# Performance work log

Measured on AMD Instinct MI355X. Metric: run time of the kernel, lower is better.

Reference implementation:

```python
import jax, jax.numpy as jnp
import numpy as np

B, C, H, W = 16, 512, 64, 64
R = 8
CP = C // R  # inner channel dim C' = 64


def setup_inputs() -> dict:
    key = jax.random.key(0)
    ks = jax.random.split(key, 10)
    s_in = 1.0 / np.sqrt(C)
    s_cp = 1.0 / np.sqrt(CP)
    return {
        "x": jax.random.normal(ks[0], (B, C, H, W), dtype=jnp.float32),
        "wq": jax.random.uniform(ks[1], (CP, C), jnp.float32, -s_in, s_in),
        "bq": jax.random.uniform(ks[2], (CP,), jnp.float32, -s_in, s_in),
        "wk": jax.random.uniform(ks[3], (CP, C), jnp.float32, -s_in, s_in),
        "bk": jax.random.uniform(ks[4], (CP,), jnp.float32, -s_in, s_in),
        "wv": jax.random.uniform(ks[5], (CP, C), jnp.float32, -s_in, s_in),
        "bv": jax.random.uniform(ks[6], (CP,), jnp.float32, -s_in, s_in),
        "wo": jax.random.uniform(ks[7], (C, CP), jnp.float32, -s_cp, s_cp),
        "bo": jax.random.uniform(ks[8], (C,), jnp.float32, -s_cp, s_cp),
        # torch init is gamma=0 (output==x, zero grads to convs); use small
        # nonzero value so the reference exercises the full graph.
        "gamma": jax.random.normal(ks[9], (1,), dtype=jnp.float32) * 0.1,
    }


def reference(x, wq, bq, wk, bk, wv, bv, wo, bo, gamma):
    b, c, h, w = x.shape
    n = h * w
    xf = x.reshape(b, c, n)  # flatten spatial -> (B, C, N)
    # 1x1 convs == channel matmuls
    q = jnp.einsum("oc,bcn->bon", wq, xf) + bq[:, None]  # (B, C', N)
    k = jnp.einsum("oc,bcn->bon", wk, xf) + bk[:, None]  # (B, C', N)
    v = jnp.einsum("oc,bcn->bon", wv, xf) + bv[:, None]  # (B, C', N)
    # energy = bmm(key (B,C',N), query^T (B,N,C')) -> (B, C', C')
    energy = jnp.einsum("bin,bjn->bij", k, q)
    attention = jax.nn.softmax(energy, axis=-1)  # (B, C', C')
    out = jnp.einsum("bij,bjn->bin", attention, v)  # (B, C', N)
    out = jnp.einsum("co,bon->bcn", wo, out) + bo[:, None]  # (B, C, N)
    out = out.reshape(b, c, h, w)
    return gamma * out + x
```

## Files before the change

kernel.cpp:

```cpp
#include <hip/hip_runtime.h>


#define NN 4096
#define CIN 512
#define CPD 64

typedef short s8v __attribute__((ext_vector_type(8)));
typedef float f4v __attribute__((ext_vector_type(4)));
typedef unsigned short u16;

__device__ __forceinline__ u16 f2bf(float f) {
    union { float f; unsigned int u; } c; c.f = f;
    unsigned int r = c.u + 0x7FFFu + ((c.u >> 16) & 1u);
    return (u16)(r >> 16);
}

__global__ __launch_bounds__(256) void k_prep(
    const float* __restrict__ wq, const float* __restrict__ wk,
    const float* __restrict__ wv, const float* __restrict__ wo,
    u16* __restrict__ wqkvb, u16* __restrict__ wob)
{
    const int t = blockIdx.x * 256 + threadIdx.x;
    const int i4 = t * 4;
    const float* src; u16* dst; int off;
    if (i4 < 98304) {
        const int r = i4 >> 15;
        src = (r == 0) ? wq : (r == 1) ? wk : wv;
        off = i4 & 32767;
        dst = wqkvb + (r << 15);
    } else {
        src = wo; off = i4 - 98304; dst = wob;
    }
    float4 v = *(const float4*)(src + off);
    u16 tmp[4] = { f2bf(v.x), f2bf(v.y), f2bf(v.z), f2bf(v.w) };
    *(uint2*)(dst + off) = *(const uint2*)tmp;
}

__global__ __launch_bounds__(256, 2) void k_qkv(
    const float* __restrict__ x,
    const u16* __restrict__ wqkvb,
    const float* __restrict__ bq, const float* __restrict__ bk,
    const float* __restrict__ bv,
    u16* __restrict__ q, u16* __restrict__ k, u16* __restrict__ vt)
{
    const int nb = blockIdx.x, b = blockIdx.y;
    const int t = threadIdx.x;
    const int wv_ = t >> 6, L = t & 63, quad = L >> 4, l15 = L & 15;

    const int n_col0 = nb * 128 + wv_ * 32 + l15;
    const size_t xbase = (size_t)b * CIN * NN;

    f4v acc[12][2];
    #pragma unroll
    for (int ot = 0; ot < 12; ++ot)
        #pragma unroll
        for (int nn = 0; nn < 2; ++nn) acc[ot][nn] = (f4v){0.f,0.f,0.f,0.f};

    for (int ks = 0; ks < 16; ++ks) {
        const int c = ks * 32 + quad * 8;
        float bx0[8], bx1[8];
        #pragma unroll
        for (int j = 0; j < 8; ++j) {
            const float* xc = x + xbase + (size_t)(c + j) * NN + n_col0;
            bx0[j] = xc[0];
            bx1[j] = xc[16];
        }
        s8v bf0, bf1;
        #pragma unroll
        for (int j = 0; j < 8; ++j) {
            bf0[j] = (short)f2bf(bx0[j]);
            bf1[j] = (short)f2bf(bx1[j]);
        }
        #pragma unroll
        for (int ot = 0; ot < 12; ++ot) {
            s8v af = *(const s8v*)(wqkvb + (ot * 16 + l15) * CIN + c);
            acc[ot][0] = __builtin_amdgcn_mfma_f32_16x16x32_bf16(
                af, bf0, acc[ot][0], 0, 0, 0);
            acc[ot][1] = __builtin_amdgcn_mfma_f32_16x16x32_bf16(
                af, bf1, acc[ot][1], 0, 0, 0);
        }
    }

    #pragma unroll
    for (int p = 0; p < 2; ++p) {
        u16* outp = ((p == 0) ? q : k) + (size_t)b * CPD * NN;
        const float* bp = (p == 0) ? bq : bk;
        #pragma unroll
        for (int ot4 = 0; ot4 < 4; ++ot4) {
            float4 b4 = *(const float4*)(bp + ot4 * 16 + quad * 4);
            const float bsv[4] = { b4.x, b4.y, b4.z, b4.w };
            #pragma unroll
            for (int nn = 0; nn < 2; ++nn) {
                const int n = n_col0 + nn * 16;
                #pragma unroll
                for (int r = 0; r < 4; ++r) {
                    int o = ot4 * 16 + quad * 4 + r;
                    outp[(size_t)o * NN + n] =
                        f2bf(acc[p * 4 + ot4][nn][r] + bsv[r]);
                }
            }
        }
    }
    {
        u16* vtb = vt + (size_t)b * NN * CPD;
        #pragma unroll
        for (int ot4 = 0; ot4 < 4; ++ot4) {
            float4 b4 = *(const float4*)(bv + ot4 * 16 + quad * 4);
            const float bsv[4] = { b4.x, b4.y, b4.z, b4.w };
            #pragma unroll
            for (int nn = 0; nn < 2; ++nn) {
                const int n = n_col0 + nn * 16;
                u16 tmp[4];
                #pragma unroll
                for (int r = 0; r < 4; ++r)
                    tmp[r] = f2bf(acc[8 + ot4][nn][r] + bsv[r]);
                *(uint2*)(vtb + (size_t)n * CPD + ot4 * 16 + quad * 4) =
                    *(const uint2*)tmp;
            }
        }
    }
}

__global__ __launch_bounds__(256, 4) void k_energy(
    const u16* __restrict__ q, const u16* __restrict__ k,
    float* __restrict__ epart)
{
    const int s = blockIdx.x;
    const int b = blockIdx.y;
    const int t = threadIdx.x;
    const int wv_ = t >> 6, L = t & 63, quad = L >> 4, l15 = L & 15;
    const u16* kb = k + (size_t)b * CPD * NN;
    const u16* qb = q + (size_t)b * CPD * NN;

    f4v acc[4][4];
    #pragma unroll
    for (int a = 0; a < 4; ++a)
        #pragma unroll
        for (int d = 0; d < 4; ++d) acc[a][d] = (f4v){0.f,0.f,0.f,0.f};

    const int nbase = s * 256 + wv_ * 64;
    #pragma unroll
    for (int ksl = 0; ksl < 2; ++ksl) {
        const int n = nbase + ksl * 32 + quad * 8;
        s8v af[4], bf_[4];
        #pragma unroll
        for (int it = 0; it < 4; ++it)
            af[it] = *(const s8v*)(kb + (size_t)(it * 16 + l15) * NN + n);
        #pragma unroll
        for (int jt = 0; jt < 4; ++jt)
            bf_[jt] = *(const s8v*)(qb + (size_t)(jt * 16 + l15) * NN + n);
        #pragma unroll
        for (int it = 0; it < 4; ++it)
            #pragma unroll
            for (int jt = 0; jt < 4; ++jt)
                acc[it][jt] = __builtin_amdgcn_mfma_f32_16x16x32_bf16(
                    af[it], bf_[jt], acc[it][jt], 0, 0, 0);
    }

    float* ep = epart + ((size_t)b * 64 + s * 4 + wv_) * 4096;
    #pragma unroll
    for (int it = 0; it < 4; ++it)
        #pragma unroll
        for (int jt = 0; jt < 4; ++jt)
            #pragma unroll
            for (int r = 0; r < 4; ++r)
                ep[(it * 16 + quad * 4 + r) * 64 + jt * 16 + l15] =
                    acc[it][jt][r];
}

__global__ __launch_bounds__(64) void k_softmax(
    const float* __restrict__ epart, u16* __restrict__ attn)
{
    const int i = blockIdx.x;
    const int b = blockIdx.y;
    const int j = threadIdx.x;
    float s = 0.f;
    #pragma unroll
    for (int sp = 0; sp < 64; ++sp)
        s += epart[((size_t)b * 64 + sp) * 4096 + i * 64 + j];
    float m = s;
    #pragma unroll
    for (int off = 32; off; off >>= 1) m = fmaxf(m, __shfl_xor(m, off));
    float e = __expf(s - m);
    float tot = e;
    #pragma unroll
    for (int off = 32; off; off >>= 1) tot += __shfl_xor(tot, off);
    attn[(size_t)b * 4096 + i * 64 + j] = f2bf(e / tot);
}

__global__ __launch_bounds__(256, 4) void k_avout(
    const u16* __restrict__ vt, const u16* __restrict__ attn,
    const u16* __restrict__ wob, const float* __restrict__ bo,
    const float* __restrict__ gamma, const float* __restrict__ x,
    float* __restrict__ out)
{
    const int nb = blockIdx.x, b = blockIdx.y;
    const int t = threadIdx.x;
    const int wv_ = t >> 6, L = t & 63, quad = L >> 4, l15 = L & 15;
    const int swz = (l15 & 7) * 8;

    __shared__ u16 avl[128 * 64];

    {
        const u16* ab  = attn + (size_t)b * 4096;
        const u16* vtb = vt + (size_t)b * NN * CPD;
        const int n0 = nb * 128;
        f4v acc1[4][2];
        #pragma unroll
        for (int a = 0; a < 4; ++a)
            #pragma unroll
            for (int d = 0; d < 2; ++d) acc1[a][d] = (f4v){0.f,0.f,0.f,0.f};
        #pragma unroll
        for (int ks = 0; ks < 2; ++ks) {
            const int j = ks * 32 + quad * 8;
            s8v af[4], bf_[2];
            #pragma unroll
            for (int it = 0; it < 4; ++it)
                af[it] = *(const s8v*)(ab + (size_t)(it * 16 + l15) * 64 + j);
            #pragma unroll
            for (int nn = 0; nn < 2; ++nn)
                bf_[nn] = *(const s8v*)(vtb +
                    (size_t)(n0 + wv_ * 32 + nn * 16 + l15) * CPD + j);
            #pragma unroll
            for (int it = 0; it < 4; ++it)
                #pragma unroll
                for (int nn = 0; nn < 2; ++nn)
                    acc1[it][nn] = __builtin_amdgcn_mfma_f32_16x16x32_bf16(
                        af[it], bf_[nn], acc1[it][nn], 0, 0, 0);
        }
        #pragma unroll
        for (int it = 0; it < 4; ++it)
            #pragma unroll
            for (int nn = 0; nn < 2; ++nn) {
                const int nloc = wv_ * 32 + nn * 16 + l15;
                u16 tmp[4];
                #pragma unroll
                for (int r = 0; r < 4; ++r) tmp[r] = f2bf(acc1[it][nn][r]);
                *(uint2*)&avl[nloc * 64 + ((it * 16 + quad * 4) ^ swz)] =
                    *(const uint2*)tmp;
            }
    }
    __syncthreads();

    const float g = gamma[0];
    const int n0 = nb * 128;
    for (int cb = 0; cb < 8; ++cb) {
        f4v acc2[2][4];
        #pragma unroll
        for (int a = 0; a < 2; ++a)
            #pragma unroll
            for (int d = 0; d < 4; ++d) acc2[a][d] = (f4v){0.f,0.f,0.f,0.f};
        #pragma unroll
        for (int ks = 0; ks < 2; ++ks) {
            const int i0 = ks * 32 + quad * 8;
            const int ic = i0 ^ swz;
            s8v af2[2], bf2[4];
            #pragma unroll
            for (int nt = 0; nt < 2; ++nt)
                af2[nt] = *(const s8v*)&avl[(wv_ * 32 + nt * 16 + l15) * 64 + ic];
            #pragma unroll
            for (int ct = 0; ct < 4; ++ct)
                bf2[ct] = *(const s8v*)(wob +
                    (size_t)(cb * 64 + ct * 16 + l15) * CPD + i0);
            #pragma unroll
            for (int nt = 0; nt < 2; ++nt)
                #pragma unroll
                for (int ct = 0; ct < 4; ++ct)
                    acc2[nt][ct] = __builtin_amdgcn_mfma_f32_16x16x32_bf16(
                        af2[nt], bf2[ct], acc2[nt][ct], 0, 0, 0);
        }
        #pragma unroll
        for (int nt = 0; nt < 2; ++nt)
            #pragma unroll
            for (int ct = 0; ct < 4; ++ct) {
                const int c = cb * 64 + ct * 16 + l15;
                const float bs = bo[c];
                const int nbase = n0 + wv_ * 32 + nt * 16 + quad * 4;
                const size_t idx = ((size_t)b * CIN + c) * NN + nbase;
                float4 xr = *(const float4*)(x + idx);
                float4 r4;
                r4.x = g * (acc2[nt][ct][0] + bs) + xr.x;
                r4.y = g * (acc2[nt][ct][1] + bs) + xr.y;
                r4.z = g * (acc2[nt][ct][2] + bs) + xr.z;
                r4.w = g * (acc2[nt][ct][3] + bs) + xr.w;
                *(float4*)(out + idx) = r4;
            }
    }
}

extern "C" void kernel_launch(void* const* d_in, const int* in_sizes, int n_in,
                              void* d_out, int out_size, void* d_ws, size_t ws_size,
                              hipStream_t stream) {
    const float* x  = (const float*)d_in[0];
    const float* wq = (const float*)d_in[1];
    const float* bq = (const float*)d_in[2];
    const float* wk = (const float*)d_in[3];
    const float* bk = (const float*)d_in[4];
    const float* wv = (const float*)d_in[5];
    const float* bv = (const float*)d_in[6];
    const float* wo = (const float*)d_in[7];
    const float* bo = (const float*)d_in[8];
    const float* gm = (const float*)d_in[9];
    float* out = (float*)d_out;

    char* wsb = (char*)d_ws;
    u16*   q     = (u16*)wsb;
    u16*   k     = (u16*)(wsb + 8388608);
    u16*   vt    = (u16*)(wsb + 16777216);
    float* epart = (float*)(wsb + 25165824);
    u16*   attn  = (u16*)(wsb + 41943040);
    u16*   wqkvb = (u16*)(wsb + 42074112);
    u16*   wob   = (u16*)(wsb + 42270720);

    k_prep<<<128, 256, 0, stream>>>(wq, wk, wv, wo, wqkvb, wob);
    k_qkv<<<dim3(32, 16), 256, 0, stream>>>(x, wqkvb, bq, bk, bv, q, k, vt);
    k_energy<<<dim3(16, 16), 256, 0, stream>>>(q, k, epart);
    k_softmax<<<dim3(64, 16), 64, 0, stream>>>(epart, attn);
    k_avout<<<dim3(32, 16), 256, 0, stream>>>(vt, attn, wob, bo, gm, x, out);
}
```

Baseline: 355.4 us.

## Pre-transpose x to bf16 channel-last and retile QKV projection

Adds a kernel that converts x to bf16 and transposes it to (B, N, C) through LDS with a swizzle. The QKV kernel can then load contiguous 16-byte MFMA operands instead of doing scalar strided fp32 loads with in-loop conversion. It is also retiled so each wave owns one 16-row output slice across q, k and v, with more blocks and higher occupancy. Separately, the energy kernel now covers twice the spatial range per block, halving the partial sums the softmax must reduce. The cost is an extra pass that writes and re-reads a 64 MB bf16 copy of x, plus a larger workspace.

New measurement: 387.1 us. 1.09x slower.

```diff
diff --git a/kernel.cpp b/kernel.cpp
--- a/kernel.cpp
+++ b/kernel.cpp
@@ -36,87 +36,105 @@
     *(uint2*)(dst + off) = *(const uint2*)tmp;
 }
 
-__global__ __launch_bounds__(256, 2) void k_qkv(
-    const float* __restrict__ x,
-    const u16* __restrict__ wqkvb,
+__global__ __launch_bounds__(256) void k_xt(
+    const float* __restrict__ x, u16* __restrict__ xt)
+{
+    const int ct = blockIdx.x, nt = blockIdx.y, b = blockIdx.z;
+    const int t = threadIdx.x;
+    const int c0 = ct * 64, n0 = nt * 64;
+    __shared__ u16 lt[64 * 64];
+
+    #pragma unroll
+    for (int p = 0; p < 4; ++p) {
+        const int c_l = p * 16 + (t >> 4);
+        const int n4  = (t & 15) * 4;
+        float4 v = *(const float4*)(x + ((size_t)b * CIN + c0 + c_l) * NN + n0 + n4);
+        u16 tmp[4] = { f2bf(v.x), f2bf(v.y), f2bf(v.z), f2bf(v.w) };
+        *(uint2*)&lt[c_l * 64 + (n4 ^ ((c_l >> 3) << 3))] = *(const uint2*)tmp;
+    }
+    __syncthreads();
+
+    #pragma unroll
+    for (int pp = 0; pp < 2; ++pp) {
+        const int n_l = pp * 32 + (t >> 3);
+        const int cg  = (t & 7) * 8;
+        const int swz = (t & 7) << 3;
+        u16 tmp[8];
+        #pragma unroll
+        for (int i = 0; i < 8; ++i)
+            tmp[i] = lt[(cg + i) * 64 + (n_l ^ swz)];
+        *(uint4*)(xt + ((size_t)b * NN + n0 + n_l) * CIN + c0 + cg) =
+            *(const uint4*)tmp;
+    }
+}
+
+__global__ __launch_bounds__(256, 4) void k_qkv(
+    const u16* __restrict__ xt, const u16* __restrict__ wqkvb,
     const float* __restrict__ bq, const float* __restrict__ bk,
     const float* __restrict__ bv,
     u16* __restrict__ q, u16* __restrict__ k, u16* __restrict__ vt)
 {
     const int nb = blockIdx.x, b = blockIdx.y;
     const int t = threadIdx.x;
-    const int wv_ = t >> 6, L = t & 63, quad = L >> 4, l15 = L & 15;
-
-    const int n_col0 = nb * 128 + wv_ * 32 + l15;
-    const size_t xbase = (size_t)b * CIN * NN;
-
-    f4v acc[12][2];
-    #pragma unroll
-    for (int ot = 0; ot < 12; ++ot)
-        #pragma unroll
-        for (int nn = 0; nn < 2; ++nn) acc[ot][nn] = (f4v){0.f,0.f,0.f,0.f};
-
+    const int w = t >> 6, L = t & 63, quad = L >> 4, l15 = L & 15;
+    const int n0 = nb * 64;
+
+    f4v acc[3][4];
+    #pragma unroll
+    for (int p = 0; p < 3; ++p)
+        #pragma unroll
+        for (int nn = 0; nn < 4; ++nn) acc[p][nn] = (f4v){0.f,0.f,0.f,0.f};
+
+    const u16* xb = xt + ((size_t)b * NN + n0) * CIN;
+    const u16* wb = wqkvb + (size_t)(w * 16 + l15) * CIN;
+
+    #pragma unroll
     for (int ks = 0; ks < 16; ++ks) {
         const int c = ks * 32 + quad * 8;
-        float bx0[8], bx1[8];
-        #pragma unroll
-        for (int j = 0; j < 8; ++j) {
-            const float* xc = x + xbase + (size_t)(c + j) * NN + n_col0;
-            bx0[j] = xc[0];
-            bx1[j] = xc[16];
-        }
-        s8v bf0, bf1;
-        #pragma unroll
-        for (int j = 0; j < 8; ++j) {
-            bf0[j] = (short)f2bf(bx0[j]);
-            bf1[j] = (short)f2bf(bx1[j]);
-        }
-        #pragma unroll
-        for (int ot = 0; ot < 12; ++ot) {
-            s8v af = *(const s8v*)(wqkvb + (ot * 16 + l15) * CIN + c);
-            acc[ot][0] = __builtin_amdgcn_mfma_f32_16x16x32_bf16(
-                af, bf0, acc[ot][0], 0, 0, 0);
-            acc[ot][1] = __builtin_amdgcn_mfma_f32_16x16x32_bf16(
-                af, bf1, acc[ot][1], 0, 0, 0);
-        }
-    }
-
-    #pragma unroll
-    for (int p = 0; p < 2; ++p) {
-        u16* outp = ((p == 0) ? q : k) + (size_t)b * CPD * NN;
-        const float* bp = (p == 0) ? bq : bk;
-        #pragma unroll
-        for (int ot4 = 0; ot4 < 4; ++ot4) {
-            float4 b4 = *(const float4*)(bp + ot4 * 16 + quad * 4);
-            const float bsv[4] = { b4.x, b4.y, b4.z, b4.w };
-            #pragma unroll
-            for (int nn = 0; nn < 2; ++nn) {
-                const int n = n_col0 + nn * 16;
-                #pragma unroll
-                for (int r = 0; r < 4; ++r) {
-                    int o = ot4 * 16 + quad * 4 + r;
-                    outp[(size_t)o * NN + n] =
-                        f2bf(acc[p * 4 + ot4][nn][r] + bsv[r]);
-                }
+        s8v bf[4], af[3];
+        #pragma unroll
+        for (int nn = 0; nn < 4; ++nn)
+            bf[nn] = *(const s8v*)(xb + (size_t)(nn * 16 + l15) * CIN + c);
+        #pragma unroll
+        for (int p = 0; p < 3; ++p)
+            af[p] = *(const s8v*)(wb + (size_t)p * 64 * CIN + c);
+        #pragma unroll
+        for (int p = 0; p < 3; ++p)
+            #pragma unroll
+            for (int nn = 0; nn < 4; ++nn)
+                acc[p][nn] = __builtin_amdgcn_mfma_f32_16x16x32_bf16(
+                    af[p], bf[nn], acc[p][nn], 0, 0, 0);
+    }
+
+    const int orow = w * 16 + quad * 4;
+    {
+        float4 q4 = *(const float4*)(bq + orow);
+        float4 k4 = *(const float4*)(bk + orow);
+        const float qb_[4] = { q4.x, q4.y, q4.z, q4.w };
+        const float kb_[4] = { k4.x, k4.y, k4.z, k4.w };
+        u16* qp = q + (size_t)b * CPD * NN;
+        u16* kp = k + (size_t)b * CPD * NN;
+        #pragma unroll
+        for (int nn = 0; nn < 4; ++nn) {
+            const int n = n0 + nn * 16 + l15;
+            #pragma unroll
+            for (int r = 0; r < 4; ++r) {
+                qp[(size_t)(orow + r) * NN + n] = f2bf(acc[0][nn][r] + qb_[r]);
+                kp[(size_t)(orow + r) * NN + n] = f2bf(acc[1][nn][r] + kb_[r]);
             }
         }
     }
     {
+        float4 v4 = *(const float4*)(bv + orow);
+        const float vb_[4] = { v4.x, v4.y, v4.z, v4.w };
         u16* vtb = vt + (size_t)b * NN * CPD;
         #pragma unroll
-        for (int ot4 = 0; ot4 < 4; ++ot4) {
-            float4 b4 = *(const float4*)(bv + ot4 * 16 + quad * 4);
-            const float bsv[4] = { b4.x, b4.y, b4.z, b4.w };
-            #pragma unroll
-            for (int nn = 0; nn < 2; ++nn) {
-                const int n = n_col0 + nn * 16;
-                u16 tmp[4];
-                #pragma unroll
-                for (int r = 0; r < 4; ++r)
-                    tmp[r] = f2bf(acc[8 + ot4][nn][r] + bsv[r]);
-                *(uint2*)(vtb + (size_t)n * CPD + ot4 * 16 + quad * 4) =
-                    *(const uint2*)tmp;
-            }
+        for (int nn = 0; nn < 4; ++nn) {
+            const int n = n0 + nn * 16 + l15;
+            u16 tmp[4];
+            #pragma unroll
+            for (int r = 0; r < 4; ++r) tmp[r] = f2bf(acc[2][nn][r] + vb_[r]);
+            *(uint2*)(vtb + (size_t)n * CPD + orow) = *(const uint2*)tmp;
         }
     }
 }
@@ -138,9 +156,9 @@
         #pragma unroll
         for (int d = 0; d < 4; ++d) acc[a][d] = (f4v){0.f,0.f,0.f,0.f};
 
-    const int nbase = s * 256 + wv_ * 64;
-    #pragma unroll
-    for (int ksl = 0; ksl < 2; ++ksl) {
+    const int nbase = s * 512 + wv_ * 128;
+    #pragma unroll
+    for (int ksl = 0; ksl < 4; ++ksl) {
         const int n = nbase + ksl * 32 + quad * 8;
         s8v af[4], bf_[4];
         #pragma unroll
@@ -157,7 +175,7 @@
                     af[it], bf_[jt], acc[it][jt], 0, 0, 0);
     }
 
-    float* ep = epart + ((size_t)b * 64 + s * 4 + wv_) * 4096;
+    float* ep = epart + ((size_t)b * 32 + s * 4 + wv_) * 4096;
     #pragma unroll
     for (int it = 0; it < 4; ++it)
         #pragma unroll
@@ -176,8 +194,8 @@
     const int j = threadIdx.x;
     float s = 0.f;
     #pragma unroll
-    for (int sp = 0; sp < 64; ++sp)
-        s += epart[((size_t)b * 64 + sp) * 4096 + i * 64 + j];
+    for (int sp = 0; sp < 32; ++sp)
+        s += epart[((size_t)b * 32 + sp) * 4096 + i * 64 + j];
     float m = s;
     #pragma unroll
     for (int off = 32; off; off >>= 1) m = fmaxf(m, __shfl_xor(m, off));
@@ -304,17 +322,19 @@
     float* out = (float*)d_out;
 
     char* wsb = (char*)d_ws;
-    u16*   q     = (u16*)wsb;
-    u16*   k     = (u16*)(wsb + 8388608);
-    u16*   vt    = (u16*)(wsb + 16777216);
-    float* epart = (float*)(wsb + 25165824);
-    u16*   attn  = (u16*)(wsb + 41943040);
-    u16*   wqkvb = (u16*)(wsb + 42074112);
-    u16*   wob   = (u16*)(wsb + 42270720);
+    u16*   xt    = (u16*)wsb;
+    u16*   q     = (u16*)(wsb + 67108864);
+    u16*   k     = (u16*)(wsb + 75497472);
+    u16*   vt    = (u16*)(wsb + 83886080);
+    float* epart = (float*)(wsb + 92274688);
+    u16*   attn  = (u16*)(wsb + 100663296);
+    u16*   wqkvb = (u16*)(wsb + 100794368);
+    u16*   wob   = (u16*)(wsb + 100990976);
 
     k_prep<<<128, 256, 0, stream>>>(wq, wk, wv, wo, wqkvb, wob);
-    k_qkv<<<dim3(32, 16), 256, 0, stream>>>(x, wqkvb, bq, bk, bv, q, k, vt);
-    k_energy<<<dim3(16, 16), 256, 0, stream>>>(q, k, epart);
+    k_xt<<<dim3(8, 64, 16), 256, 0, stream>>>(x, xt);
+    k_qkv<<<dim3(64, 16), 256, 0, stream>>>(xt, wqkvb, bq, bk, bv, q, k, vt);
+    k_energy<<<dim3(8, 16), 256, 0, stream>>>(q, k, epart);
     k_softmax<<<dim3(64, 16), 64, 0, stream>>>(epart, attn);
     k_avout<<<dim3(32, 16), 256, 0, stream>>>(vt, attn, wob, bo, gm, x, out);
 }
```
